# Performance work log

Hardware: AMD Instinct MI355X
Metric: run time of the kernel (lower is better)

The kernel has to match this reference:

```python
import jax, jax.numpy as jnp
import numpy as np

N = 65536      # tokens
D = 512        # input_dim
H = 8          # num_heads
HD = 64        # head_dim
FF = 2048      # hidden_dim
EPS = 1e-5


def _layer_norm(x, g, b):
    mu = jnp.mean(x, axis=-1, keepdims=True)
    var = jnp.mean(jnp.square(x - mu), axis=-1, keepdims=True)
    return (x - mu) * jax.lax.rsqrt(var + EPS) * g + b


def setup_inputs() -> dict:
    key = jax.random.key(0)
    ks = jax.random.split(key, 12)
    s_d = 1.0 / np.sqrt(D)
    s_f = 1.0 / np.sqrt(FF)
    return {
        "x":   jax.random.normal(ks[0], (N, D), jnp.float32),
        # Linear weights stored [in, out] (transpose of torch's [out, in])
        "Wq":  jax.random.uniform(ks[1], (D, D), jnp.float32, -s_d, s_d),
        "bq":  jnp.zeros((D,), jnp.float32),
        "Wk":  jax.random.uniform(ks[2], (D, D), jnp.float32, -s_d, s_d),
        "bk":  jnp.zeros((D,), jnp.float32),
        "Wv":  jax.random.uniform(ks[3], (D, D), jnp.float32, -s_d, s_d),
        "bv":  jnp.zeros((D,), jnp.float32),
        "ln1_g": jnp.ones((D,), jnp.float32),
        "ln1_b": jnp.zeros((D,), jnp.float32),
        "W1":  jax.random.uniform(ks[4], (D, FF), jnp.float32, -s_d, s_d),
        "b1":  jnp.zeros((FF,), jnp.float32),
        "W2":  jax.random.uniform(ks[5], (FF, D), jnp.float32, -s_f, s_f),
        "b2":  jnp.zeros((D,), jnp.float32),
        "ln2_g": jnp.ones((D,), jnp.float32),
        "ln2_b": jnp.zeros((D,), jnp.float32),
    }


def reference(x, Wq, bq, Wk, bk, Wv, bv, ln1_g, ln1_b, W1, b1, W2, b2, ln2_g, ln2_b):
    n = x.shape[0]
    # --- multi-head attention (per-token head mixing, as in source) ---
    q = (x @ Wq + bq).reshape(n, H, HD)
    k = (x @ Wk + bk).reshape(n, H, HD)
    v = (x @ Wv + bv).reshape(n, H, HD)
    # score[n] = q[n] @ k[n]^T : [H, H] per token
    score = jnp.einsum("nhd,ngd->nhg", q, k) / jnp.sqrt(jnp.float32(HD))
    attn = jax.nn.softmax(score, axis=-1)
    ctx = jnp.einsum("nhg,ngd->nhd", attn, v).reshape(n, D)
    y = _layer_norm(x + ctx, ln1_g, ln1_b)
    # --- feed forward with residual + layer norm ---
    h = jax.nn.relu(y @ W1 + b1)
    z = h @ W2 + b2 + y
    return _layer_norm(z, ln2_g, ln2_b)
```

## Files before the change

kernel.cpp:

```cpp
#include <hip/hip_runtime.h>
#include <cstdint>


typedef __attribute__((ext_vector_type(8))) short bf16x8;
typedef __attribute__((ext_vector_type(4))) float f32x4;
typedef __attribute__((ext_vector_type(8))) unsigned short u16x8;

__device__ __forceinline__ float bf2f(unsigned short u) {
  union { unsigned int i; float f; } v; v.i = ((unsigned int)u) << 16; return v.f;
}
__device__ __forceinline__ unsigned short f2bf(float f) {
  union { float f; unsigned int i; } v; v.f = f;
  unsigned int r = v.i + 0x7FFFu + ((v.i >> 16) & 1u);
  return (unsigned short)(r >> 16);
}

#define GLD16(g, l)                                                         \
  __builtin_amdgcn_global_load_lds(                                         \
      (const __attribute__((address_space(1))) void*)(g),                   \
      (__attribute__((address_space(3))) void*)(l), 16, 0, 0)

__global__ __launch_bounds__(256) void cast_f32_bf16(
    const float* __restrict__ in, ushort* __restrict__ out) {
  const size_t i = (size_t)blockIdx.x * 256 + threadIdx.x;
  const float4* p = (const float4*)in + i * 2;
  float4 a = p[0], b = p[1];
  u16x8 r;
  r[0] = f2bf(a.x); r[1] = f2bf(a.y); r[2] = f2bf(a.z); r[3] = f2bf(a.w);
  r[4] = f2bf(b.x); r[5] = f2bf(b.y); r[6] = f2bf(b.z); r[7] = f2bf(b.w);
  ((u16x8*)out)[i] = r;
}

__global__ __launch_bounds__(256) void transpose_cast(
    const float* __restrict__ W, ushort* __restrict__ Wt,
    int K, int Nn, int rowoff, int ldt) {
  __shared__ float tile[32][33];
  const int tx = threadIdx.x & 31, ty = threadIdx.x >> 5;
  const int nb = blockIdx.x * 32, kb = blockIdx.y * 32;
#pragma unroll
  for (int s = 0; s < 4; ++s)
    tile[ty + 8 * s][tx] = W[(size_t)(kb + ty + 8 * s) * Nn + nb + tx];
  __syncthreads();
#pragma unroll
  for (int s = 0; s < 4; ++s)
    Wt[(size_t)(rowoff + nb + ty + 8 * s) * ldt + kb + tx] =
        f2bf(tile[tx][ty + 8 * s]);
}

template <int EPI>
__global__ __launch_bounds__(512, 2) void gemm_bt(
    const ushort* __restrict__ A, const ushort* __restrict__ Bt,
    int N, int K, void* __restrict__ Cout,
    const float* __restrict__ bias0, const float* __restrict__ bias1,
    const float* __restrict__ bias2, const ushort* __restrict__ resid) {
  constexpr int BK = 32;
  __shared__ __align__(16) ushort lds[4 * 16384];
  const int tid = threadIdx.x;
  const int wid = tid >> 6, lane = tid & 63;
  const int wm = wid >> 2, wn = wid & 3;
  const size_t m0 = (size_t)blockIdx.y * 256;
  const size_t n0 = (size_t)blockIdx.x * 256;
  const int NT = K / BK;

  const int sgcol = (((tid & 3) - ((tid >> 3) & 3)) & 3) << 3;
  const ushort* a0 = A + (m0 + (tid >> 2)) * (size_t)K + sgcol;
  const ushort* b0 = Bt + (n0 + (tid >> 2)) * (size_t)K + sgcol;
  const size_t rowK = 128 * (size_t)K;
  ushort* ldst = &lds[tid * 8];

#define STAGE_T(t)                                                          \
  {                                                                         \
    ushort* d = ldst + ((t) & 3) * 16384;                                   \
    const ushort* ga = a0 + (size_t)(t) * BK;                               \
    const ushort* gb = b0 + (size_t)(t) * BK;                               \
    GLD16(ga, d);                                                           \
    GLD16(ga + rowK, d + 4096);                                             \
    GLD16(gb, d + 8192);                                                    \
    GLD16(gb + rowK, d + 12288);                                            \
  }

  const int cswz = ((((lane >> 4) + ((lane >> 1) & 3)) & 3) << 3);
  const int arow = wm * 128 + (lane & 15);
  const int brow = wn * 64 + (lane & 15);

  f32x4 acc[8][4] = {};

  STAGE_T(0);
  STAGE_T(1);
  STAGE_T(2);

  for (int t = 0; t < NT; ++t) {
    if (t < NT - 2) {
      asm volatile("s_waitcnt vmcnt(8)" ::: "memory");
    } else if (t == NT - 2) {
      asm volatile("s_waitcnt vmcnt(4)" ::: "memory");
    } else {
      asm volatile("s_waitcnt vmcnt(0)" ::: "memory");
    }
    __builtin_amdgcn_s_barrier();

    const ushort* lA = &lds[(t & 3) * 16384];
    const ushort* lB = lA + 8192;

    if (t + 3 < NT) STAGE_T(t + 3);

    bf16x8 af[8], bfr[4];
#pragma unroll
    for (int mi = 0; mi < 8; ++mi)
      af[mi] = *(const bf16x8*)&lA[(arow + mi * 16) * 32 + cswz];
#pragma unroll
    for (int ni = 0; ni < 4; ++ni)
      bfr[ni] = *(const bf16x8*)&lB[(brow + ni * 16) * 32 + cswz];

    __builtin_amdgcn_s_setprio(1);
#pragma unroll
    for (int mi = 0; mi < 8; ++mi)
#pragma unroll
      for (int ni = 0; ni < 4; ++ni)
        acc[mi][ni] = __builtin_amdgcn_mfma_f32_16x16x32_bf16(
            af[mi], bfr[ni], acc[mi][ni], 0, 0, 0);
    __builtin_amdgcn_s_setprio(0);
  }
#undef STAGE_T

  const int lm = lane & 15, lq = lane >> 4;
#pragma unroll
  for (int ni = 0; ni < 4; ++ni) {
    const size_t col = n0 + wn * 64 + ni * 16 + lm;
    float bv;
    if (EPI == 0) {
      const float* bp = (n0 < 512) ? bias0 : ((n0 < 1024) ? bias1 : bias2);
      bv = bp[col & 511];
    } else {
      bv = bias0[col];
    }
#pragma unroll
    for (int mi = 0; mi < 8; ++mi) {
#pragma unroll
      for (int j = 0; j < 4; ++j) {
        const size_t row = m0 + wm * 128 + mi * 16 + lq * 4 + j;
        float v = acc[mi][ni][j] + bv;
        if (EPI == 0) {
          ((ushort*)Cout)[row * N + col] = f2bf(v);
        } else if (EPI == 1) {
          ((ushort*)Cout)[row * N + col] = f2bf(fmaxf(v, 0.f));
        } else {
          v += bf2f(resid[row * N + col]);
          ((float*)Cout)[row * N + col] = v;
        }
      }
    }
  }
}

__global__ __launch_bounds__(256) void attn_ln1(
    const ushort* __restrict__ qkv, const float* __restrict__ x,
    const float* __restrict__ g1, const float* __restrict__ b1,
    ushort* __restrict__ y) {
  const int lane = threadIdx.x & 63;
  const size_t t = (size_t)blockIdx.x * 4 + (threadIdx.x >> 6);
  const ushort* base = qkv + t * 1536;
  float qd[8], kd[8], vd[8];
#pragma unroll
  for (int h = 0; h < 8; ++h) {
    qd[h] = bf2f(base[h * 64 + lane]);
    kd[h] = bf2f(base[512 + h * 64 + lane]);
    vd[h] = bf2f(base[1024 + h * 64 + lane]);
  }

  const bool lb0 = lane & 1, lb1 = lane & 2, lb2 = lane & 4;
  const bool lb3 = lane & 8, lb4 = lane & 16, lb5 = lane & 32;

  float c1[32];
#pragma unroll
  for (int f = 0; f < 32; ++f) {
    const int i0 = 2 * f, i1 = 2 * f + 1;
    const float a0 = qd[i0 >> 3] * kd[i0 & 7];
    const float a1 = qd[i1 >> 3] * kd[i1 & 7];
    const float keep = lb0 ? a1 : a0;
    const float send = lb0 ? a0 : a1;
    c1[f] = keep + __shfl_xor(send, 1, 64);
  }
  float c2[16];
#pragma unroll
  for (int f = 0; f < 16; ++f) {
    const float keep = lb1 ? c1[2 * f + 1] : c1[2 * f];
    const float send = lb1 ? c1[2 * f] : c1[2 * f + 1];
    c2[f] = keep + __shfl_xor(send, 2, 64);
  }
  float c3[8];
#pragma unroll
  for (int f = 0; f < 8; ++f) {
    const float keep = lb2 ? c2[2 * f + 1] : c2[2 * f];
    const float send = lb2 ? c2[2 * f] : c2[2 * f + 1];
    c3[f] = keep + __shfl_xor(send, 4, 64);
  }
  float c4[4];
#pragma unroll
  for (int f = 0; f < 4; ++f) {
    const float keep = lb3 ? c3[2 * f + 1] : c3[2 * f];
    const float send = lb3 ? c3[2 * f] : c3[2 * f + 1];
    c4[f] = keep + __shfl_xor(send, 8, 64);
  }
  float c5[2];
#pragma unroll
  for (int f = 0; f < 2; ++f) {
    const float keep = lb4 ? c4[2 * f + 1] : c4[2 * f];
    const float send = lb4 ? c4[2 * f] : c4[2 * f + 1];
    c5[f] = keep + __shfl_xor(send, 16, 64);
  }
  const float keep = lb5 ? c5[1] : c5[0];
  const float send = lb5 ? c5[0] : c5[1];
  const float s = keep + __shfl_xor(send, 32, 64);

  float mx = s;
  mx = fmaxf(mx, __shfl_xor(mx, 1, 64));
  mx = fmaxf(mx, __shfl_xor(mx, 2, 64));
  mx = fmaxf(mx, __shfl_xor(mx, 4, 64));
  const float e = __expf((s - mx) * 0.125f);
  float sum = e;
  sum += __shfl_xor(sum, 1, 64);
  sum += __shfl_xor(sum, 2, 64);
  sum += __shfl_xor(sum, 4, 64);
  const float a = e * __builtin_amdgcn_rcpf(sum);

  const int ai = __float_as_int(a);
  float r[8];
#pragma unroll
  for (int h = 0; h < 8; ++h) {
    float c = 0.f;
#pragma unroll
    for (int g = 0; g < 8; ++g) {
      const float w = __int_as_float(__builtin_amdgcn_readlane(ai, h * 8 + g));
      c = fmaf(w, vd[g], c);
    }
    r[h] = x[t * 512 + h * 64 + lane] + c;
  }

  float sm = 0.f, sq = 0.f;
#pragma unroll
  for (int h = 0; h < 8; ++h) { sm += r[h]; sq += r[h] * r[h]; }
#pragma unroll
  for (int m = 1; m < 64; m <<= 1) {
    sm += __shfl_xor(sm, m, 64);
    sq += __shfl_xor(sq, m, 64);
  }
  const float mu = sm * (1.f / 512.f);
  const float var = sq * (1.f / 512.f) - mu * mu;
  const float rs = rsqrtf(var + 1e-5f);
#pragma unroll
  for (int h = 0; h < 8; ++h) {
    const int d = h * 64 + lane;
    y[t * 512 + d] = f2bf((r[h] - mu) * rs * g1[d] + b1[d]);
  }
}

__global__ __launch_bounds__(256) void ln_out(
    const float* __restrict__ z, const float* __restrict__ g2,
    const float* __restrict__ b2, float* __restrict__ out) {
  const int lane = threadIdx.x & 63;
  const size_t t = (size_t)blockIdx.x * 4 + (threadIdx.x >> 6);
  const float4* zp = (const float4*)(z + t * 512);
  const float4 r0 = zp[lane], r1 = zp[lane + 64];
  float sm = r0.x + r0.y + r0.z + r0.w + r1.x + r1.y + r1.z + r1.w;
  float sq = r0.x * r0.x + r0.y * r0.y + r0.z * r0.z + r0.w * r0.w +
             r1.x * r1.x + r1.y * r1.y + r1.z * r1.z + r1.w * r1.w;
#pragma unroll
  for (int m = 1; m < 64; m <<= 1) {
    sm += __shfl_xor(sm, m, 64);
    sq += __shfl_xor(sq, m, 64);
  }
  const float mu = sm * (1.f / 512.f);
  const float rs = rsqrtf(sq * (1.f / 512.f) - mu * mu + 1e-5f);
  const float4* g4 = (const float4*)g2;
  const float4* b4 = (const float4*)b2;
  float4* o4 = (float4*)(out + t * 512);
  const float4 ga = g4[lane], gb = g4[lane + 64];
  const float4 ba = b4[lane], bb = b4[lane + 64];
  float4 oa, ob;
  oa.x = (r0.x - mu) * rs * ga.x + ba.x;
  oa.y = (r0.y - mu) * rs * ga.y + ba.y;
  oa.z = (r0.z - mu) * rs * ga.z + ba.z;
  oa.w = (r0.w - mu) * rs * ga.w + ba.w;
  ob.x = (r1.x - mu) * rs * gb.x + bb.x;
  ob.y = (r1.y - mu) * rs * gb.y + bb.y;
  ob.z = (r1.z - mu) * rs * gb.z + bb.z;
  ob.w = (r1.w - mu) * rs * gb.w + bb.w;
  o4[lane] = oa;
  o4[lane + 64] = ob;
}

extern "C" void kernel_launch(void* const* d_in, const int* in_sizes, int n_in,
                              void* d_out, int out_size, void* d_ws,
                              size_t ws_size, hipStream_t stream) {
  const float* x    = (const float*)d_in[0];
  const float* Wq   = (const float*)d_in[1];
  const float* bq   = (const float*)d_in[2];
  const float* Wk   = (const float*)d_in[3];
  const float* bk   = (const float*)d_in[4];
  const float* Wv   = (const float*)d_in[5];
  const float* bv   = (const float*)d_in[6];
  const float* ln1g = (const float*)d_in[7];
  const float* ln1b = (const float*)d_in[8];
  const float* W1   = (const float*)d_in[9];
  const float* b1   = (const float*)d_in[10];
  const float* W2   = (const float*)d_in[11];
  const float* b2   = (const float*)d_in[12];
  const float* ln2g = (const float*)d_in[13];
  const float* ln2b = (const float*)d_in[14];
  float* out = (float*)d_out;

  const int Ntok = in_sizes[0] / 512;

  char* ws = (char*)d_ws;
  ushort* Wqkvt = (ushort*)ws;
  ushort* W1t   = Wqkvt + (size_t)1536 * 512;
  ushort* W2t   = W1t + (size_t)2048 * 512;
  const size_t woff = ((size_t)1536 * 512 + (size_t)2048 * 512 +
                       (size_t)512 * 2048) * 2;

  size_t avail = (ws_size > woff) ? (ws_size - woff) : 0;
  long long Cll = (long long)(avail / 9216);
  Cll = (Cll / 256) * 256;
  if (Cll > 32768) Cll = 32768;
  if (Cll > Ntok) Cll = Ntok;
  if (Cll < 256) Cll = 256;
  const int C = (int)Cll;

  char* cb = ws + woff;
  ushort* xb  = (ushort*)cb;
  ushort* y   = xb + (size_t)C * 512;
  ushort* qkv = y + (size_t)C * 512;
  ushort* hb  = qkv + (size_t)C * 1536;
  float*  z   = (float*)qkv;

  transpose_cast<<<dim3(16, 16), dim3(256), 0, stream>>>(Wq, Wqkvt, 512, 512, 0, 512);
  transpose_cast<<<dim3(16, 16), dim3(256), 0, stream>>>(Wk, Wqkvt, 512, 512, 512, 512);
  transpose_cast<<<dim3(16, 16), dim3(256), 0, stream>>>(Wv, Wqkvt, 512, 512, 1024, 512);
  transpose_cast<<<dim3(64, 16), dim3(256), 0, stream>>>(W1, W1t, 512, 2048, 0, 512);
  transpose_cast<<<dim3(16, 64), dim3(256), 0, stream>>>(W2, W2t, 2048, 512, 0, 2048);

  for (int t0 = 0; t0 < Ntok; t0 += C) {
    const int Cc = (Ntok - t0 < C) ? (Ntok - t0) : C;
    const float* xc = x + (size_t)t0 * 512;

    cast_f32_bf16<<<dim3((Cc * 512) / 2048), dim3(256), 0, stream>>>(xc, xb);

    gemm_bt<0><<<dim3(1536 / 256, Cc / 256), dim3(512), 0, stream>>>(
        xb, Wqkvt, 1536, 512, qkv, bq, bk, bv, nullptr);

    attn_ln1<<<dim3(Cc / 4), dim3(256), 0, stream>>>(qkv, xc, ln1g, ln1b, y);

    gemm_bt<1><<<dim3(2048 / 256, Cc / 256), dim3(512), 0, stream>>>(
        y, W1t, 2048, 512, hb, b1, nullptr, nullptr, nullptr);

    gemm_bt<2><<<dim3(512 / 256, Cc / 256), dim3(512), 0, stream>>>(
        hb, W2t, 512, 2048, z, b2, nullptr, nullptr, y);

    ln_out<<<dim3(Cc / 4), dim3(256), 0, stream>>>(
        z, ln2g, ln2b, out + (size_t)t0 * 512);
  }
}
```

Measured before the change: 780.9 us.

## Split GEMM k-step into two half-phases, swizzle blocks across XCDs, reorder epilogue

Each k-iteration now runs as two phases: the first loads half the A fragments plus the B fragments and issues the A global-to-LDS prefetch, and the second, after an extra barrier, loads the other A half and issues the B prefetch. This interleaves memory traffic with MFMA work and lowers register pressure from fragment arrays. Workgroup IDs are remapped so consecutive tiles land on the same XCD, aiming for better L2 reuse. The epilogue hoists the bias loads and reorders the store loops. The extra barrier per iteration adds synchronisation cost.

```diff
diff --git a/kernel.cpp b/kernel.cpp
--- a/kernel.cpp
+++ b/kernel.cpp
@@ -58,8 +58,16 @@
   const int tid = threadIdx.x;
   const int wid = tid >> 6, lane = tid & 63;
   const int wm = wid >> 2, wn = wid & 3;
-  const size_t m0 = (size_t)blockIdx.y * 256;
-  const size_t n0 = (size_t)blockIdx.x * 256;
+
+  const int gx = gridDim.x;
+  const int nwg = gx * gridDim.y;
+  const int orig = blockIdx.y * gx + blockIdx.x;
+  const int q = nwg >> 3, r = nwg & 7;
+  const int xcd = orig & 7, loc = orig >> 3;
+  const int swz = (xcd < r) ? (xcd * (q + 1) + loc)
+                            : (r * (q + 1) + (xcd - r) * q + loc);
+  const size_t m0 = (size_t)(swz / gx) * 256;
+  const size_t n0 = (size_t)(swz % gx) * 256;
   const int NT = K / BK;
 
   const int sgcol = (((tid & 3) - ((tid >> 3) & 3)) & 3) << 3;
@@ -68,15 +76,19 @@
   const size_t rowK = 128 * (size_t)K;
   ushort* ldst = &lds[tid * 8];
 
-#define STAGE_T(t)                                                          \
+#define STAGE_A(t)                                                          \
   {                                                                         \
     ushort* d = ldst + ((t) & 3) * 16384;                                   \
-    const ushort* ga = a0 + (size_t)(t) * BK;                               \
-    const ushort* gb = b0 + (size_t)(t) * BK;                               \
-    GLD16(ga, d);                                                           \
-    GLD16(ga + rowK, d + 4096);                                             \
-    GLD16(gb, d + 8192);                                                    \
-    GLD16(gb + rowK, d + 12288);                                            \
+    const ushort* g = a0 + (size_t)(t) * BK;                                \
+    GLD16(g, d);                                                            \
+    GLD16(g + rowK, d + 4096);                                              \
+  }
+#define STAGE_B(t)                                                          \
+  {                                                                         \
+    ushort* d = ldst + ((t) & 3) * 16384 + 8192;                            \
+    const ushort* g = b0 + (size_t)(t) * BK;                                \
+    GLD16(g, d);                                                            \
+    GLD16(g + rowK, d + 4096);                                              \
   }
 
   const int cswz = ((((lane >> 4) + ((lane >> 1) & 3)) & 3) << 3);
@@ -85,9 +97,9 @@
 
   f32x4 acc[8][4] = {};
 
-  STAGE_T(0);
-  STAGE_T(1);
-  STAGE_T(2);
+  STAGE_A(0); STAGE_B(0);
+  STAGE_A(1); STAGE_B(1);
+  STAGE_A(2); STAGE_B(2);
 
   for (int t = 0; t < NT; ++t) {
     if (t < NT - 2) {
@@ -102,51 +114,69 @@
     const ushort* lA = &lds[(t & 3) * 16384];
     const ushort* lB = lA + 8192;
 
-    if (t + 3 < NT) STAGE_T(t + 3);
-
-    bf16x8 af[8], bfr[4];
-#pragma unroll
-    for (int mi = 0; mi < 8; ++mi)
+    bf16x8 af[4], bfr[4];
+#pragma unroll
+    for (int mi = 0; mi < 4; ++mi)
       af[mi] = *(const bf16x8*)&lA[(arow + mi * 16) * 32 + cswz];
 #pragma unroll
     for (int ni = 0; ni < 4; ++ni)
       bfr[ni] = *(const bf16x8*)&lB[(brow + ni * 16) * 32 + cswz];
-
+    if (t + 3 < NT) STAGE_A(t + 3);
     __builtin_amdgcn_s_setprio(1);
 #pragma unroll
-    for (int mi = 0; mi < 8; ++mi)
+    for (int mi = 0; mi < 4; ++mi)
 #pragma unroll
       for (int ni = 0; ni < 4; ++ni)
         acc[mi][ni] = __builtin_amdgcn_mfma_f32_16x16x32_bf16(
             af[mi], bfr[ni], acc[mi][ni], 0, 0, 0);
     __builtin_amdgcn_s_setprio(0);
-  }
-#undef STAGE_T
+    __builtin_amdgcn_s_barrier();
+
+    bf16x8 ag[4];
+#pragma unroll
+    for (int mi = 0; mi < 4; ++mi)
+      ag[mi] = *(const bf16x8*)&lA[(arow + (mi + 4) * 16) * 32 + cswz];
+    if (t + 3 < NT) STAGE_B(t + 3);
+    __builtin_amdgcn_s_setprio(1);
+#pragma unroll
+    for (int mi = 0; mi < 4; ++mi)
+#pragma unroll
+      for (int ni = 0; ni < 4; ++ni)
+        acc[mi + 4][ni] = __builtin_amdgcn_mfma_f32_16x16x32_bf16(
+            ag[mi], bfr[ni], acc[mi + 4][ni], 0, 0, 0);
+    __builtin_amdgcn_s_setprio(0);
+  }
+#undef STAGE_A
+#undef STAGE_B
 
   const int lm = lane & 15, lq = lane >> 4;
+  size_t col[4];
+  float bv[4];
 #pragma unroll
   for (int ni = 0; ni < 4; ++ni) {
-    const size_t col = n0 + wn * 64 + ni * 16 + lm;
-    float bv;
+    col[ni] = n0 + wn * 64 + ni * 16 + lm;
     if (EPI == 0) {
       const float* bp = (n0 < 512) ? bias0 : ((n0 < 1024) ? bias1 : bias2);
-      bv = bp[col & 511];
+      bv[ni] = bp[col[ni] & 511];
     } else {
-      bv = bias0[col];
+      bv[ni] = bias0[col[ni]];
     }
-#pragma unroll
-    for (int mi = 0; mi < 8; ++mi) {
-#pragma unroll
-      for (int j = 0; j < 4; ++j) {
-        const size_t row = m0 + wm * 128 + mi * 16 + lq * 4 + j;
-        float v = acc[mi][ni][j] + bv;
+  }
+#pragma unroll
+  for (int mi = 0; mi < 8; ++mi) {
+#pragma unroll
+    for (int j = 0; j < 4; ++j) {
+      const size_t row = m0 + wm * 128 + mi * 16 + lq * 4 + j;
+#pragma unroll
+      for (int ni = 0; ni < 4; ++ni) {
+        float v = acc[mi][ni][j] + bv[ni];
         if (EPI == 0) {
-          ((ushort*)Cout)[row * N + col] = f2bf(v);
+          ((ushort*)Cout)[row * N + col[ni]] = f2bf(v);
         } else if (EPI == 1) {
-          ((ushort*)Cout)[row * N + col] = f2bf(fmaxf(v, 0.f));
+          ((ushort*)Cout)[row * N + col[ni]] = f2bf(fmaxf(v, 0.f));
         } else {
-          v += bf2f(resid[row * N + col]);
-          ((float*)Cout)[row * N + col] = v;
+          v += bf2f(resid[row * N + col[ni]]);
+          ((float*)Cout)[row * N + col[ni]] = v;
         }
       }
     }
```

After: 666.8 us. 1.17x faster.
